# Kernel optimization log

Measured on AMD Instinct MI355X. Metric: run time of the kernel, lower is better.

## Reference

```python
import jax, jax.numpy as jnp
import numpy as np

N_NODES = 50000
NEG_SLOPE = 0.2  # DGL GATConv default


def _leaky_relu(x):
    return jnp.where(x >= 0, x, NEG_SLOPE * x)


def gat_conv(h, W, al, ar, src, dst, activate):
    # h: [N, F_in], W: [F_in, H, D], al/ar: [H, D]
    fs = jnp.einsum('nf,fhd->nhd', h, W)          # [N, H, D]
    el = jnp.sum(fs * al, axis=-1)                 # [N, H]
    er = jnp.sum(fs * ar, axis=-1)                 # [N, H]
    e = _leaky_relu(el[src] + er[dst])             # [E, H]
    # numerically stable edge softmax per destination node
    m = jax.ops.segment_max(e, dst, num_segments=N_NODES)   # [N, H]
    ex = jnp.exp(e - m[dst])                                  # [E, H]
    s = jax.ops.segment_sum(ex, dst, num_segments=N_NODES)  # [N, H]
    alpha = ex / s[dst]                                       # [E, H]
    msg = alpha[:, :, None] * fs[src]                          # [E, H, D]
    out = jax.ops.segment_sum(msg, dst, num_segments=N_NODES) # [N, H, D]
    if activate:
        out = jax.nn.relu(out)
    return out


def setup_inputs() -> dict:
    key = jax.random.key(0)
    ks = jax.random.split(key, 12)
    E = 1600000
    H, D, Fin, C = 4, 32, 100, 47
    inp = {
        'x': jax.random.normal(ks[0], (N_NODES, Fin), jnp.float32),
        'W0': jax.random.normal(ks[1], (Fin, H, D), jnp.float32) * 0.1,
        'al0': jax.random.normal(ks[2], (H, D), jnp.float32) * 0.1,
        'ar0': jax.random.normal(ks[3], (H, D), jnp.float32) * 0.1,
        'W1': jax.random.normal(ks[4], (H * D, H, D), jnp.float32) * 0.1,
        'al1': jax.random.normal(ks[5], (H, D), jnp.float32) * 0.1,
        'ar1': jax.random.normal(ks[6], (H, D), jnp.float32) * 0.1,
        'W2': jax.random.normal(ks[7], (H * D, H, C), jnp.float32) * 0.1,
        'al2': jax.random.normal(ks[8], (H, C), jnp.float32) * 0.1,
        'ar2': jax.random.normal(ks[9], (H, C), jnp.float32) * 0.1,
        'src': jax.random.randint(ks[10], (E,), 0, N_NODES, jnp.int32),
        'dst': jax.random.randint(ks[11], (E,), 0, N_NODES, jnp.int32),
    }
    return inp


def reference(x, W0, al0, ar0, W1, al1, ar1, W2, al2, ar2, src, dst):
    h = gat_conv(x, W0, al0, ar0, src, dst, True)            # [N, H, D]
    h = h.reshape(h.shape[0], -1)                             # flatten(1)
    h = gat_conv(h, W1, al1, ar1, src, dst, True)
    h = h.reshape(h.shape[0], -1)
    h = gat_conv(h, W2, al2, ar2, src, dst, False)           # [N, H, C]
    h = h.mean(axis=1)                                        # mean over heads
    return jax.nn.log_softmax(h, axis=-1)                     # [N, C]
```

## Files before the change

### kernel.cpp

```cpp
#include <hip/hip_runtime.h>
#include <hip/hip_bf16.h>


using bf16 = __hip_bfloat16;
typedef __attribute__((ext_vector_type(8))) short short8;
typedef __attribute__((ext_vector_type(4))) float floatx4;

static constexpr int NN = 50000;
static constexpr int H  = 4;

__device__ __forceinline__ float b2f(bf16 x) { return __bfloat162float(x); }
__device__ __forceinline__ float ldx(const void* p, size_t i, bool bf) {
    return bf ? __bfloat162float(((const bf16*)p)[i]) : ((const float*)p)[i];
}
__device__ __forceinline__ unsigned short f2b_bits(float v) {
    bf16 h = __float2bfloat16(v);
    return *reinterpret_cast<unsigned short*>(&h);
}
__device__ __forceinline__ unsigned short w_bits(const void* p, size_t i, bool bf) {
    if (bf) return ((const unsigned short*)p)[i];
    return f2b_bits(((const float*)p)[i]);
}
__device__ __forceinline__ float bl(unsigned u) { return __uint_as_float(u << 16); }
__device__ __forceinline__ float bh(unsigned u) { return __uint_as_float(u & 0xFFFF0000u); }

__global__ void detect_k(const void* __restrict__ x, int* __restrict__ flag) {
    __shared__ int cnt;
    if (threadIdx.x == 0) cnt = 0;
    __syncthreads();
    const unsigned short* u = (const unsigned short*)x;
    unsigned short b = u[threadIdx.x * 2];
    int e = (b >> 7) & 0xFF;
    if (e >= 0x70 && e <= 0x8F) atomicAdd(&cnt, 1);
    __syncthreads();
    if (threadIdx.x == 0) *flag = (cnt > 128) ? 1 : 0;
}

__global__ void zero_i_k(int* __restrict__ p, int n) {
    int i = blockIdx.x * 256 + threadIdx.x;
    if (i < n) p[i] = 0;
}

__global__ void deg_k(const int* __restrict__ dst, int* __restrict__ deg, int E) {
    int e = blockIdx.x * 256 + threadIdx.x;
    if (e < E) atomicAdd(&deg[dst[e]], 1);
}

__global__ void scan1_k(const int* __restrict__ deg, int* __restrict__ rowptr,
                        int* __restrict__ bsum, int N) {
    __shared__ int buf[256];
    int tid = threadIdx.x, i = blockIdx.x * 256 + tid;
    int v = (i < N) ? deg[i] : 0;
    buf[tid] = v;
    __syncthreads();
    for (int off = 1; off < 256; off <<= 1) {
        int t = (tid >= off) ? buf[tid - off] : 0;
        __syncthreads();
        buf[tid] += t;
        __syncthreads();
    }
    if (i < N) rowptr[i] = buf[tid] - v;
    if (tid == 255) bsum[blockIdx.x] = buf[255];
}

__global__ void scan2_k(const int* __restrict__ bsum, int* __restrict__ boff, int nb) {
    __shared__ int buf[256];
    int tid = threadIdx.x;
    int v = (tid < nb) ? bsum[tid] : 0;
    buf[tid] = v;
    __syncthreads();
    for (int off = 1; off < 256; off <<= 1) {
        int t = (tid >= off) ? buf[tid - off] : 0;
        __syncthreads();
        buf[tid] += t;
        __syncthreads();
    }
    if (tid < nb) boff[tid] = buf[tid] - v;
}

__global__ void scan3_k(int* __restrict__ rowptr, const int* __restrict__ boff,
                        int N, int E) {
    int i = blockIdx.x * 256 + threadIdx.x;
    if (i < N) rowptr[i] += boff[blockIdx.x];
    if (i == 0) rowptr[N] = E;
}

__global__ void fill_k(const int* __restrict__ src, const int* __restrict__ dst,
                       const int* __restrict__ rowptr, int* __restrict__ cur,
                       int* __restrict__ col, int E) {
    int e = blockIdx.x * 256 + threadIdx.x;
    if (e >= E) return;
    int d = dst[e];
    int p = atomicAdd(&cur[d], 1);
    col[rowptr[d] + p] = src[e];
}

template <int K, int M, int S, int HD, int IN_MODE>
__global__ void __launch_bounds__(256) gemm_k(const void* __restrict__ in,
                                              const void* __restrict__ W,
                                              const void* __restrict__ al,
                                              const void* __restrict__ ar,
                                              bf16* __restrict__ fs,
                                              float* __restrict__ el,
                                              float* __restrict__ er,
                                              const int* __restrict__ flag, int N) {
    constexpr int KP  = 128;
    constexpr int CT  = S / 16;
    constexpr int WST = 136;
    __shared__ short wlds[S * WST];
    const bool bf = (*flag != 0);
    const int tid = threadIdx.x;

    for (int idx = tid; idx < (KP / 2) * M; idx += 256) {
        int k2 = idx / M, c = idx % M;
        int k0 = 2 * k2;
        unsigned short u0 = (k0 < K)     ? w_bits(W, (size_t)k0 * M + c, bf)       : 0;
        unsigned short u1 = (k0 + 1 < K) ? w_bits(W, (size_t)(k0 + 1) * M + c, bf) : 0;
        *(unsigned*)&wlds[c * WST + 2 * k2] = (unsigned)u0 | ((unsigned)u1 << 16);
    }
    if (S > M) {
        for (int idx = tid; idx < (S - M) * (KP / 2); idx += 256) {
            int c = M + idx / (KP / 2);
            int k2 = idx % (KP / 2);
            *(unsigned*)&wlds[c * WST + 2 * k2] = 0u;
        }
    }
    __syncthreads();

    const int wave = tid >> 6, lane = tid & 63;
    const int q = lane >> 4, l16 = lane & 15;
    const int tile_base = blockIdx.x * 64 + wave * 16;
    const int node_a = tile_base + l16;

    floatx4 acc[CT] = {};

#pragma unroll
    for (int chunk = 0; chunk < 4; ++chunk) {
        const int kb = chunk * 32 + q * 8;
        short8 a = {};
        if (IN_MODE == 0) {
#pragma unroll
            for (int j = 0; j < 8; ++j) {
                int k = kb + j;
                float v = (node_a < N && k < K) ? ldx(in, (size_t)node_a * K + k, bf) : 0.f;
                a[j] = (short)f2b_bits(v);
            }
        } else {
            if (node_a < N)
                a = *(const short8*)((const bf16*)in + (size_t)node_a * K + kb);
        }
#pragma unroll
        for (int ct = 0; ct < CT; ++ct) {
            const int c = ct * 16 + l16;
            short8 b = *(const short8*)&wlds[c * WST + kb];
            acc[ct] = __builtin_amdgcn_mfma_f32_16x16x32_bf16(a, b, acc[ct], 0, 0, 0);
        }
    }

#pragma unroll
    for (int ct = 0; ct < CT; ++ct) {
        const int c = ct * 16 + l16;
#pragma unroll
        for (int r = 0; r < 4; ++r) {
            int node = tile_base + q * 4 + r;
            if (node < N) fs[(size_t)node * S + c] = __float2bfloat16(acc[ct][r]);
        }
    }

    __syncthreads();
    float* red = (float*)wlds;
    float elp[4][4] = {}, erp[4][4] = {};
#pragma unroll
    for (int ct = 0; ct < CT; ++ct) {
        const int c = ct * 16 + l16;
        float alc = (c < M) ? ldx(al, c, bf) : 0.f;
        float arc = (c < M) ? ldx(ar, c, bf) : 0.f;
        const int h = (c < M) ? (c / HD) : 3;
#pragma unroll
        for (int r = 0; r < 4; ++r) {
            float v = acc[ct][r];
#pragma unroll
            for (int h2 = 0; h2 < 4; ++h2) {
                elp[r][h2] += (h == h2) ? v * alc : 0.f;
                erp[r][h2] += (h == h2) ? v * arc : 0.f;
            }
        }
    }
#pragma unroll
    for (int r = 0; r < 4; ++r)
#pragma unroll
        for (int h2 = 0; h2 < 4; ++h2) {
            int slot = (wave * 128) + (q * 32) + (r * 8) + (h2 * 2);
            red[slot * 16 + l16] = elp[r][h2];
            red[(slot + 1) * 16 + l16] = erp[r][h2];
        }
    __syncthreads();
#pragma unroll
    for (int pass = 0; pass < 2; ++pass) {
        int slot = tid + pass * 256;
        float sum = 0.f;
#pragma unroll
        for (int j = 0; j < 16; ++j) sum += red[slot * 16 + j];
        int which = slot & 1;
        int h2 = (slot >> 1) & 3;
        int r  = (slot >> 3) & 3;
        int qq = (slot >> 5) & 3;
        int wv = slot >> 7;
        int node = blockIdx.x * 64 + wv * 16 + qq * 4 + r;
        if (node < N) {
            if (which == 0) el[(size_t)node * 4 + h2] = sum;
            else            er[(size_t)node * 4 + h2] = sum;
        }
    }
}

template <int D, int S, int LPG, int TPB, bool RELU, bool OUT_BF>
__global__ void __launch_bounds__(TPB) agg_k(const float* __restrict__ el,
                                             const float* __restrict__ er,
                                             const bf16* __restrict__ fs,
                                             const int* __restrict__ rowptr,
                                             const int* __restrict__ col,
                                             void* __restrict__ out) {
    constexpr int NG = TPB / LPG;
    constexpr int CH = TPB / 4;
    constexpr int NW = TPB / 64;
    const int d = blockIdx.x;
    const int tid = threadIdx.x;
    const int rs = rowptr[d], re = rowptr[d + 1];

    __shared__ float wrow[CH][4];
    __shared__ int scol_s[CH];
    __shared__ float part[NG][S];
    __shared__ float red2[NW][4];
    __shared__ float sh_s[4];

    if (re == rs) {
        if (tid < S / 4) {
            if (OUT_BF) *(uint2*)((bf16*)out + (size_t)d * S + tid * 4) = make_uint2(0, 0);
            else        *(float4*)((float*)out + (size_t)d * S + tid * 4) = make_float4(0, 0, 0, 0);
        }
        return;
    }

    float4 er4 = *(const float4*)(er + (size_t)d * 4);
    float er_d[4] = {er4.x, er4.y, er4.z, er4.w};

    const int g  = tid / LPG;
    const int lg = tid % LPG;
    const int c0 = lg * 8;
    const int ha = (c0) / D > 3 ? 3 : (c0) / D;
    const int hb = (c0 + 7) / D > 3 ? 3 : (c0 + 7) / D;
    bool kb_mask[8];
#pragma unroll
    for (int k = 0; k < 8; ++k) kb_mask[k] = (((c0 + k) / D > 3 ? 3 : (c0 + k) / D) != ha);

    float acc[8] = {0, 0, 0, 0, 0, 0, 0, 0};
    float swpart = 0.f;

    for (int cs = rs; cs < re; cs += CH) {
        int ne = min(CH, re - cs);
        if (tid < ne * 4) {
            int j = tid >> 2, h = tid & 3;
            int s = col[cs + j];
            if (h == 0) scol_s[j] = s;
            float x = el[(size_t)s * 4 + h] + er_d[h];
            x = x >= 0.f ? x : 0.2f * x;
            float w = __expf(x);
            wrow[j][h] = w;
            swpart += w;
        }
        __syncthreads();
#pragma unroll 4
        for (int e = g; e < ne; e += NG) {
            int s = scol_s[e];
            uint4 u = *(const uint4*)(fs + (size_t)s * S + c0);
            float wa = wrow[e][ha];
            float wb = (hb == ha) ? wa : wrow[e][hb];
            float f[8];
            f[0] = bl(u.x); f[1] = bh(u.x);
            f[2] = bl(u.y); f[3] = bh(u.y);
            f[4] = bl(u.z); f[5] = bh(u.z);
            f[6] = bl(u.w); f[7] = bh(u.w);
#pragma unroll
            for (int k = 0; k < 8; ++k) acc[k] += (kb_mask[k] ? wb : wa) * f[k];
        }
        __syncthreads();
    }

    float sw = swpart;
#pragma unroll
    for (int off = 4; off < 64; off <<= 1) sw += __shfl_xor(sw, off);
    const int wave = tid >> 6, lane = tid & 63;
    if (lane < 4) red2[wave][lane] = sw;
#pragma unroll
    for (int k = 0; k < 8; ++k) part[g][c0 + k] = acc[k];
    __syncthreads();
    if (tid < 4) {
        float s = 0.f;
#pragma unroll
        for (int w = 0; w < NW; ++w) s += red2[w][tid];
        sh_s[tid] = s;
    }
    __syncthreads();

    if (tid < S / 4) {
        int c = tid * 4;
        float4 v = make_float4(0, 0, 0, 0);
#pragma unroll
        for (int gg = 0; gg < NG; ++gg) {
            v.x += part[gg][c + 0]; v.y += part[gg][c + 1];
            v.z += part[gg][c + 2]; v.w += part[gg][c + 3];
        }
        v.x /= sh_s[min((c + 0) / D, 3)];
        v.y /= sh_s[min((c + 1) / D, 3)];
        v.z /= sh_s[min((c + 2) / D, 3)];
        v.w /= sh_s[min((c + 3) / D, 3)];
        if (RELU) {
            v.x = fmaxf(v.x, 0.f); v.y = fmaxf(v.y, 0.f);
            v.z = fmaxf(v.z, 0.f); v.w = fmaxf(v.w, 0.f);
        }
        if (OUT_BF) {
            unsigned p0 = (unsigned)f2b_bits(v.x) | ((unsigned)f2b_bits(v.y) << 16);
            unsigned p1 = (unsigned)f2b_bits(v.z) | ((unsigned)f2b_bits(v.w) << 16);
            *(uint2*)((bf16*)out + (size_t)d * S + c) = make_uint2(p0, p1);
        } else {
            *(float4*)((float*)out + (size_t)d * S + c) = v;
        }
    }
}

__global__ void final_k(const float* __restrict__ acc, void* __restrict__ out,
                        const int* __restrict__ flag, int N) {
    int n = blockIdx.x;
    int c = threadIdx.x;
    const bool bf = (*flag != 0);
    const float* p = acc + (size_t)n * 192;
    float val = 0.f, v = -INFINITY;
    if (c < 47) {
        val = 0.25f * (p[c] + p[47 + c] + p[94 + c] + p[141 + c]);
        v = val;
    }
    float m = v;
#pragma unroll
    for (int off = 32; off >= 1; off >>= 1) m = fmaxf(m, __shfl_xor(m, off));
    float ex = (c < 47) ? __expf(val - m) : 0.f;
    float s = ex;
#pragma unroll
    for (int off = 32; off >= 1; off >>= 1) s += __shfl_xor(s, off);
    if (c < 47) {
        float r = val - m - logf(s);
        if (bf) ((bf16*)out)[(size_t)n * 47 + c] = __float2bfloat16(r);
        else    ((float*)out)[(size_t)n * 47 + c] = r;
    }
}

extern "C" void kernel_launch(void* const* d_in, const int* in_sizes, int n_in,
                              void* d_out, int out_size, void* d_ws, size_t ws_size,
                              hipStream_t stream) {
    const void* x   = d_in[0];
    const void* W0  = d_in[1];
    const void* al0 = d_in[2];
    const void* ar0 = d_in[3];
    const void* W1  = d_in[4];
    const void* al1 = d_in[5];
    const void* ar1 = d_in[6];
    const void* W2  = d_in[7];
    const void* al2 = d_in[8];
    const void* ar2 = d_in[9];
    const int* src  = (const int*)d_in[10];
    const int* dst  = (const int*)d_in[11];
    const int E = in_sizes[10];
    const int N = NN;

    bf16* fs    = (bf16*)d_ws;
    bf16* hb16  = fs + (size_t)N * 192;
    float* hbuf = (float*)(hb16 + (size_t)N * 128);
    float* el   = hbuf + (size_t)N * 192;
    float* er   = el + (size_t)N * H;
    int* rowptr = (int*)(er + (size_t)N * H);
    int* cur    = rowptr + (N + 1);
    int* col    = cur + N;
    int* bsum   = col + E;
    int* boff   = bsum + 256;
    int* flag   = boff + 256;

    const int gN = (N + 255) / 256;
    const int gE = (E + 255) / 256;
    const int gG = (N + 63) / 64;

    detect_k<<<1, 256, 0, stream>>>(x, flag);

    zero_i_k<<<gN, 256, 0, stream>>>(cur, N);
    deg_k<<<gE, 256, 0, stream>>>(dst, cur, E);
    scan1_k<<<gN, 256, 0, stream>>>(cur, rowptr, bsum, N);
    scan2_k<<<1, 256, 0, stream>>>(bsum, boff, gN);
    scan3_k<<<gN, 256, 0, stream>>>(rowptr, boff, N, E);
    zero_i_k<<<gN, 256, 0, stream>>>(cur, N);
    fill_k<<<gE, 256, 0, stream>>>(src, dst, rowptr, cur, col, E);

    gemm_k<100, 128, 128, 32, 0><<<gG, 256, 0, stream>>>(
        x, W0, al0, ar0, fs, el, er, flag, N);
    agg_k<32, 128, 16, 256, true, true><<<N, 256, 0, stream>>>(
        el, er, fs, rowptr, col, hb16);

    gemm_k<128, 128, 128, 32, 1><<<gG, 256, 0, stream>>>(
        hb16, W1, al1, ar1, fs, el, er, flag, N);
    agg_k<32, 128, 16, 256, true, true><<<N, 256, 0, stream>>>(
        el, er, fs, rowptr, col, hb16);

    gemm_k<128, 188, 192, 47, 1><<<gG, 256, 0, stream>>>(
        hb16, W2, al2, ar2, fs, el, er, flag, N);
    agg_k<47, 192, 24, 192, false, false><<<N, 192, 0, stream>>>(
        el, er, fs, rowptr, col, hbuf);

    final_k<<<N, 64, 0, stream>>>(hbuf, d_out, flag, N);
}
```

Before: 643.8 us.

## Pad layer-3 heads to 48 columns, fuse final log-softmax into aggregation, pre-pad input

Layer-3 features are laid out with each head padded to 48 columns, so every 8-column group of a lane belongs to exactly one head. This removes the per-element head mask and second weight lookup from the aggregation loop, and divisions become a multiply by a reciprocal. The last aggregation now computes the head mean and log-softmax in-kernel, removing final_k and the fp32 round-trip buffer. The input x is converted once into a 128-wide bf16 padded buffer, so the first GEMM uses vector loads; this costs an extra kernel launch and buffer write.

```diff
diff --git a/kernel.cpp b/kernel.cpp
--- a/kernel.cpp
+++ b/kernel.cpp
@@ -34,6 +34,16 @@
     if (e >= 0x70 && e <= 0x8F) atomicAdd(&cnt, 1);
     __syncthreads();
     if (threadIdx.x == 0) *flag = (cnt > 128) ? 1 : 0;
+}
+
+__global__ void xpad_k(const void* __restrict__ x, bf16* __restrict__ xp,
+                       const int* __restrict__ flag, int total) {
+    int i = blockIdx.x * 256 + threadIdx.x;
+    if (i >= total) return;
+    const bool bf = (*flag != 0);
+    int n = i >> 7, k = i & 127;
+    float v = (k < 100) ? ldx(x, (size_t)n * 100 + k, bf) : 0.f;
+    xp[i] = __float2bfloat16(v);
 }
 
 __global__ void zero_i_k(int* __restrict__ p, int n) {
@@ -95,8 +105,8 @@
     col[rowptr[d] + p] = src[e];
 }
 
-template <int K, int M, int S, int HD, int IN_MODE>
-__global__ void __launch_bounds__(256) gemm_k(const void* __restrict__ in,
+template <int KW, int M, int S, int HS, int HW>
+__global__ void __launch_bounds__(256) gemm_k(const bf16* __restrict__ in,
                                               const void* __restrict__ W,
                                               const void* __restrict__ al,
                                               const void* __restrict__ ar,
@@ -104,26 +114,21 @@
                                               float* __restrict__ el,
                                               float* __restrict__ er,
                                               const int* __restrict__ flag, int N) {
-    constexpr int KP  = 128;
     constexpr int CT  = S / 16;
     constexpr int WST = 136;
     __shared__ short wlds[S * WST];
     const bool bf = (*flag != 0);
     const int tid = threadIdx.x;
 
-    for (int idx = tid; idx < (KP / 2) * M; idx += 256) {
-        int k2 = idx / M, c = idx % M;
+    for (int idx = tid; idx < 64 * S; idx += 256) {
+        int k2 = idx / S, p = idx % S;
+        int j = p % HS, h = p / HS;
+        int c = h * HW + j;
+        bool valid = (j < HW);
         int k0 = 2 * k2;
-        unsigned short u0 = (k0 < K)     ? w_bits(W, (size_t)k0 * M + c, bf)       : 0;
-        unsigned short u1 = (k0 + 1 < K) ? w_bits(W, (size_t)(k0 + 1) * M + c, bf) : 0;
-        *(unsigned*)&wlds[c * WST + 2 * k2] = (unsigned)u0 | ((unsigned)u1 << 16);
-    }
-    if (S > M) {
-        for (int idx = tid; idx < (S - M) * (KP / 2); idx += 256) {
-            int c = M + idx / (KP / 2);
-            int k2 = idx % (KP / 2);
-            *(unsigned*)&wlds[c * WST + 2 * k2] = 0u;
-        }
+        unsigned short u0 = (valid && k0 < KW)     ? w_bits(W, (size_t)k0 * M + c, bf)       : 0;
+        unsigned short u1 = (valid && k0 + 1 < KW) ? w_bits(W, (size_t)(k0 + 1) * M + c, bf) : 0;
+        *(unsigned*)&wlds[p * WST + 2 * k2] = (unsigned)u0 | ((unsigned)u1 << 16);
     }
     __syncthreads();
 
@@ -138,32 +143,22 @@
     for (int chunk = 0; chunk < 4; ++chunk) {
         const int kb = chunk * 32 + q * 8;
         short8 a = {};
-        if (IN_MODE == 0) {
-#pragma unroll
-            for (int j = 0; j < 8; ++j) {
-                int k = kb + j;
-                float v = (node_a < N && k < K) ? ldx(in, (size_t)node_a * K + k, bf) : 0.f;
-                a[j] = (short)f2b_bits(v);
-            }
-        } else {
-            if (node_a < N)
-                a = *(const short8*)((const bf16*)in + (size_t)node_a * K + kb);
-        }
+        if (node_a < N) a = *(const short8*)(in + (size_t)node_a * 128 + kb);
 #pragma unroll
         for (int ct = 0; ct < CT; ++ct) {
-            const int c = ct * 16 + l16;
-            short8 b = *(const short8*)&wlds[c * WST + kb];
+            const int p = ct * 16 + l16;
+            short8 b = *(const short8*)&wlds[p * WST + kb];
             acc[ct] = __builtin_amdgcn_mfma_f32_16x16x32_bf16(a, b, acc[ct], 0, 0, 0);
         }
     }
 
 #pragma unroll
     for (int ct = 0; ct < CT; ++ct) {
-        const int c = ct * 16 + l16;
+        const int p = ct * 16 + l16;
 #pragma unroll
         for (int r = 0; r < 4; ++r) {
             int node = tile_base + q * 4 + r;
-            if (node < N) fs[(size_t)node * S + c] = __float2bfloat16(acc[ct][r]);
+            if (node < N) fs[(size_t)node * S + p] = __float2bfloat16(acc[ct][r]);
         }
     }
 
@@ -172,10 +167,11 @@
     float elp[4][4] = {}, erp[4][4] = {};
 #pragma unroll
     for (int ct = 0; ct < CT; ++ct) {
-        const int c = ct * 16 + l16;
-        float alc = (c < M) ? ldx(al, c, bf) : 0.f;
-        float arc = (c < M) ? ldx(ar, c, bf) : 0.f;
-        const int h = (c < M) ? (c / HD) : 3;
+        const int p = ct * 16 + l16;
+        const int j = p % HS, h = p / HS;
+        const bool valid = (j < HW);
+        float alc = valid ? ldx(al, h * HW + j, bf) : 0.f;
+        float arc = valid ? ldx(ar, h * HW + j, bf) : 0.f;
 #pragma unroll
         for (int r = 0; r < 4; ++r) {
             float v = acc[ct][r];
@@ -214,13 +210,13 @@
     }
 }
 
-template <int D, int S, int LPG, int TPB, bool RELU, bool OUT_BF>
+template <int HS, int S, int LPG, int TPB, bool RELU>
 __global__ void __launch_bounds__(TPB) agg_k(const float* __restrict__ el,
                                              const float* __restrict__ er,
                                              const bf16* __restrict__ fs,
                                              const int* __restrict__ rowptr,
                                              const int* __restrict__ col,
-                                             void* __restrict__ out) {
+                                             bf16* __restrict__ out) {
     constexpr int NG = TPB / LPG;
     constexpr int CH = TPB / 4;
     constexpr int NW = TPB / 64;
@@ -235,10 +231,7 @@
     __shared__ float sh_s[4];
 
     if (re == rs) {
-        if (tid < S / 4) {
-            if (OUT_BF) *(uint2*)((bf16*)out + (size_t)d * S + tid * 4) = make_uint2(0, 0);
-            else        *(float4*)((float*)out + (size_t)d * S + tid * 4) = make_float4(0, 0, 0, 0);
-        }
+        if (tid < S / 4) *(uint2*)(out + (size_t)d * S + tid * 4) = make_uint2(0, 0);
         return;
     }
 
@@ -248,11 +241,7 @@
     const int g  = tid / LPG;
     const int lg = tid % LPG;
     const int c0 = lg * 8;
-    const int ha = (c0) / D > 3 ? 3 : (c0) / D;
-    const int hb = (c0 + 7) / D > 3 ? 3 : (c0 + 7) / D;
-    bool kb_mask[8];
-#pragma unroll
-    for (int k = 0; k < 8; ++k) kb_mask[k] = (((c0 + k) / D > 3 ? 3 : (c0 + k) / D) != ha);
+    const int h0 = c0 / HS;
 
     float acc[8] = {0, 0, 0, 0, 0, 0, 0, 0};
     float swpart = 0.f;
@@ -274,15 +263,11 @@
         for (int e = g; e < ne; e += NG) {
             int s = scol_s[e];
             uint4 u = *(const uint4*)(fs + (size_t)s * S + c0);
-            float wa = wrow[e][ha];
-            float wb = (hb == ha) ? wa : wrow[e][hb];
-            float f[8];
-            f[0] = bl(u.x); f[1] = bh(u.x);
-            f[2] = bl(u.y); f[3] = bh(u.y);
-            f[4] = bl(u.z); f[5] = bh(u.z);
-            f[6] = bl(u.w); f[7] = bh(u.w);
-#pragma unroll
-            for (int k = 0; k < 8; ++k) acc[k] += (kb_mask[k] ? wb : wa) * f[k];
+            float w = wrow[e][h0];
+            acc[0] += w * bl(u.x); acc[1] += w * bh(u.x);
+            acc[2] += w * bl(u.y); acc[3] += w * bh(u.y);
+            acc[4] += w * bl(u.z); acc[5] += w * bh(u.z);
+            acc[6] += w * bl(u.w); acc[7] += w * bh(u.w);
         }
         __syncthreads();
     }
@@ -311,46 +296,136 @@
             v.x += part[gg][c + 0]; v.y += part[gg][c + 1];
             v.z += part[gg][c + 2]; v.w += part[gg][c + 3];
         }
-        v.x /= sh_s[min((c + 0) / D, 3)];
-        v.y /= sh_s[min((c + 1) / D, 3)];
-        v.z /= sh_s[min((c + 2) / D, 3)];
-        v.w /= sh_s[min((c + 3) / D, 3)];
+        float is = 1.0f / sh_s[c / HS];
+        v.x *= is; v.y *= is; v.z *= is; v.w *= is;
         if (RELU) {
             v.x = fmaxf(v.x, 0.f); v.y = fmaxf(v.y, 0.f);
             v.z = fmaxf(v.z, 0.f); v.w = fmaxf(v.w, 0.f);
         }
-        if (OUT_BF) {
-            unsigned p0 = (unsigned)f2b_bits(v.x) | ((unsigned)f2b_bits(v.y) << 16);
-            unsigned p1 = (unsigned)f2b_bits(v.z) | ((unsigned)f2b_bits(v.w) << 16);
-            *(uint2*)((bf16*)out + (size_t)d * S + c) = make_uint2(p0, p1);
-        } else {
-            *(float4*)((float*)out + (size_t)d * S + c) = v;
-        }
-    }
-}
-
-__global__ void final_k(const float* __restrict__ acc, void* __restrict__ out,
-                        const int* __restrict__ flag, int N) {
-    int n = blockIdx.x;
-    int c = threadIdx.x;
+        unsigned p0 = (unsigned)f2b_bits(v.x) | ((unsigned)f2b_bits(v.y) << 16);
+        unsigned p1 = (unsigned)f2b_bits(v.z) | ((unsigned)f2b_bits(v.w) << 16);
+        *(uint2*)(out + (size_t)d * S + c) = make_uint2(p0, p1);
+    }
+}
+
+__global__ void __launch_bounds__(192) agg2_k(const float* __restrict__ el,
+                                              const float* __restrict__ er,
+                                              const bf16* __restrict__ fs,
+                                              const int* __restrict__ rowptr,
+                                              const int* __restrict__ col,
+                                              void* __restrict__ out,
+                                              const int* __restrict__ flag) {
+    constexpr int HS = 48, S = 192, LPG = 24, TPB = 192;
+    constexpr int NG = TPB / LPG;
+    constexpr int CH = TPB / 4;
+    constexpr int NW = TPB / 64;
+    const int d = blockIdx.x;
+    const int tid = threadIdx.x;
     const bool bf = (*flag != 0);
-    const float* p = acc + (size_t)n * 192;
-    float val = 0.f, v = -INFINITY;
-    if (c < 47) {
-        val = 0.25f * (p[c] + p[47 + c] + p[94 + c] + p[141 + c]);
-        v = val;
-    }
-    float m = v;
-#pragma unroll
-    for (int off = 32; off >= 1; off >>= 1) m = fmaxf(m, __shfl_xor(m, off));
-    float ex = (c < 47) ? __expf(val - m) : 0.f;
-    float s = ex;
-#pragma unroll
-    for (int off = 32; off >= 1; off >>= 1) s += __shfl_xor(s, off);
-    if (c < 47) {
-        float r = val - m - logf(s);
-        if (bf) ((bf16*)out)[(size_t)n * 47 + c] = __float2bfloat16(r);
-        else    ((float*)out)[(size_t)n * 47 + c] = r;
+    const int rs = rowptr[d], re = rowptr[d + 1];
+
+    __shared__ float wrow[CH][4];
+    __shared__ int scol_s[CH];
+    __shared__ float part[NG][S];
+    __shared__ float red2[NW][4];
+    __shared__ float sh_s[4];
+    __shared__ float vout[S];
+
+    if (re == rs) {
+        if (tid < 47) {
+            float r = -logf(47.f);
+            if (bf) ((bf16*)out)[(size_t)d * 47 + tid] = __float2bfloat16(r);
+            else    ((float*)out)[(size_t)d * 47 + tid] = r;
+        }
+        return;
+    }
+
+    float4 er4 = *(const float4*)(er + (size_t)d * 4);
+    float er_d[4] = {er4.x, er4.y, er4.z, er4.w};
+
+    const int g  = tid / LPG;
+    const int lg = tid % LPG;
+    const int c0 = lg * 8;
+    const int h0 = c0 / HS;
+
+    float acc[8] = {0, 0, 0, 0, 0, 0, 0, 0};
+    float swpart = 0.f;
+
+    for (int cs = rs; cs < re; cs += CH) {
+        int ne = min(CH, re - cs);
+        if (tid < ne * 4) {
+            int j = tid >> 2, h = tid & 3;
+            int s = col[cs + j];
+            if (h == 0) scol_s[j] = s;
+            float x = el[(size_t)s * 4 + h] + er_d[h];
+            x = x >= 0.f ? x : 0.2f * x;
+            float w = __expf(x);
+            wrow[j][h] = w;
+            swpart += w;
+        }
+        __syncthreads();
+#pragma unroll 4
+        for (int e = g; e < ne; e += NG) {
+            int s = scol_s[e];
+            uint4 u = *(const uint4*)(fs + (size_t)s * S + c0);
+            float w = wrow[e][h0];
+            acc[0] += w * bl(u.x); acc[1] += w * bh(u.x);
+            acc[2] += w * bl(u.y); acc[3] += w * bh(u.y);
+            acc[4] += w * bl(u.z); acc[5] += w * bh(u.z);
+            acc[6] += w * bl(u.w); acc[7] += w * bh(u.w);
+        }
+        __syncthreads();
+    }
+
+    float sw = swpart;
+#pragma unroll
+    for (int off = 4; off < 64; off <<= 1) sw += __shfl_xor(sw, off);
+    const int wave = tid >> 6, lane = tid & 63;
+    if (lane < 4) red2[wave][lane] = sw;
+#pragma unroll
+    for (int k = 0; k < 8; ++k) part[g][c0 + k] = acc[k];
+    __syncthreads();
+    if (tid < 4) {
+        float s = 0.f;
+#pragma unroll
+        for (int w = 0; w < NW; ++w) s += red2[w][tid];
+        sh_s[tid] = s;
+    }
+    __syncthreads();
+
+    if (tid < S / 4) {
+        int c = tid * 4;
+        float4 v = make_float4(0, 0, 0, 0);
+#pragma unroll
+        for (int gg = 0; gg < NG; ++gg) {
+            v.x += part[gg][c + 0]; v.y += part[gg][c + 1];
+            v.z += part[gg][c + 2]; v.w += part[gg][c + 3];
+        }
+        float is = 1.0f / sh_s[c / HS];
+        vout[c + 0] = v.x * is; vout[c + 1] = v.y * is;
+        vout[c + 2] = v.z * is; vout[c + 3] = v.w * is;
+    }
+    __syncthreads();
+
+    if (tid < 64) {
+        int c = tid;
+        float val = 0.f, vm = -INFINITY;
+        if (c < 47) {
+            val = 0.25f * (vout[c] + vout[48 + c] + vout[96 + c] + vout[144 + c]);
+            vm = val;
+        }
+        float m = vm;
+#pragma unroll
+        for (int off = 32; off >= 1; off >>= 1) m = fmaxf(m, __shfl_xor(m, off));
+        float ex = (c < 47) ? __expf(val - m) : 0.f;
+        float s = ex;
+#pragma unroll
+        for (int off = 32; off >= 1; off >>= 1) s += __shfl_xor(s, off);
+        if (c < 47) {
+            float r = val - m - logf(s);
+            if (bf) ((bf16*)out)[(size_t)d * 47 + c] = __float2bfloat16(r);
+            else    ((float*)out)[(size_t)d * 47 + c] = r;
+        }
     }
 }
 
@@ -374,8 +449,8 @@
 
     bf16* fs    = (bf16*)d_ws;
     bf16* hb16  = fs + (size_t)N * 192;
-    float* hbuf = (float*)(hb16 + (size_t)N * 128);
-    float* el   = hbuf + (size_t)N * 192;
+    bf16* xpad  = hb16 + (size_t)N * 128;
+    float* el   = (float*)(xpad + (size_t)N * 128);
     float* er   = el + (size_t)N * H;
     int* rowptr = (int*)(er + (size_t)N * H);
     int* cur    = rowptr + (N + 1);
@@ -389,6 +464,7 @@
     const int gG = (N + 63) / 64;
 
     detect_k<<<1, 256, 0, stream>>>(x, flag);
+    xpad_k<<<(N * 128 + 255) / 256, 256, 0, stream>>>(x, xpad, flag, N * 128);
 
     zero_i_k<<<gN, 256, 0, stream>>>(cur, N);
     deg_k<<<gE, 256, 0, stream>>>(dst, cur, E);
@@ -398,20 +474,15 @@
     zero_i_k<<<gN, 256, 0, stream>>>(cur, N);
     fill_k<<<gE, 256, 0, stream>>>(src, dst, rowptr, cur, col, E);
 
-    gemm_k<100, 128, 128, 32, 0><<<gG, 256, 0, stream>>>(
-        x, W0, al0, ar0, fs, el, er, flag, N);
-    agg_k<32, 128, 16, 256, true, true><<<N, 256, 0, stream>>>(
-        el, er, fs, rowptr, col, hb16);
-
-    gemm_k<128, 128, 128, 32, 1><<<gG, 256, 0, stream>>>(
+    gemm_k<100, 128, 128, 32, 32><<<gG, 256, 0, stream>>>(
+        xpad, W0, al0, ar0, fs, el, er, flag, N);
+    agg_k<32, 128, 16, 256, true><<<N, 256, 0, stream>>>(el, er, fs, rowptr, col, hb16);
+
+    gemm_k<128, 128, 128, 32, 32><<<gG, 256, 0, stream>>>(
         hb16, W1, al1, ar1, fs, el, er, flag, N);
-    agg_k<32, 128, 16, 256, true, true><<<N, 256, 0, stream>>>(
-        el, er, fs, rowptr, col, hb16);
-
-    gemm_k<128, 188, 192, 47, 1><<<gG, 256, 0, stream>>>(
+    agg_k<32, 128, 16, 256, true><<<N, 256, 0, stream>>>(el, er, fs, rowptr, col, hb16);
+
+    gemm_k<128, 188, 192, 48, 47><<<gG, 256, 0, stream>>>(
         hb16, W2, al2, ar2, fs, el, er, flag, N);
-    agg_k<47, 192, 24, 192, false, false><<<N, 192, 0, stream>>>(
-        el, er, fs, rowptr, col, hbuf);
-
-    final_k<<<N, 64, 0, stream>>>(hbuf, d_out, flag, N);
-}
+    agg2_k<<<N, 192, 0, stream>>>(el, er, fs, rowptr, col, d_out, flag);
+}
```

New measurement: 644.6 us. Within noise of the previous version (+0.1%).
